# Optimization experiments

Hardware: AMD Instinct MI355X
Metric: run time of the kernel (lower is better)

## Reference

```python
import jax, jax.numpy as jnp
import numpy as np

N_CLUSTERS = 64
N_GHOST = 2
EPS = 1e-12  # F.normalize eps


def setup_inputs() -> dict:
    key = jax.random.key(0)
    k1, k2, k3, k4 = jax.random.split(key, 4)
    n_utts, feat_dim, duration = 16, 256, 1500
    x = jax.random.normal(k1, (n_utts, feat_dim, duration), dtype=jnp.float32)
    centroids = jax.random.uniform(k2, (N_CLUSTERS, feat_dim), dtype=jnp.float32)
    # NetVLAD init ties linear.weight = 2*alpha*centroids(+ghosts); here independent params suffice for a math baseline
    lin_w = jax.random.normal(k3, (N_CLUSTERS + N_GHOST, feat_dim), dtype=jnp.float32)
    lin_b = jax.random.normal(k4, (N_CLUSTERS + N_GHOST,), dtype=jnp.float32)
    return {"x": x, "centroids": centroids, "lin_w": lin_w, "lin_b": lin_b}


def reference(x, centroids, lin_w, lin_b):
    # x: [u, f, t] -> [u, t, f]
    n_utts = x.shape[0]
    xt = jnp.transpose(x, (0, 2, 1))
    # soft assignments over clusters+ghosts, then drop ghost columns
    logits = jnp.einsum('utf,cf->utc', xt, lin_w) + lin_b  # [u,t,C+G]
    a = jax.nn.softmax(logits, axis=2)[..., :N_CLUSTERS]   # [u,t,C]
    # Fused NetVLAD aggregation (algebraically identical to
    # sum_t a[u,t,c] * (x[u,t,:] - centroids[c,:]) without materializing
    # the [u,t,C,f] residual tensor):
    comp = jnp.einsum('utc,utf->ucf', a, xt) - a.sum(axis=1)[..., None] * centroids  # [u,C,f]
    # intra-normalization (F.normalize p=2 over feat dim)
    comp = comp / jnp.maximum(jnp.linalg.norm(comp, axis=2, keepdims=True), EPS)
    sv = comp.reshape(n_utts, -1)  # [u, C*f]
    sv = sv / jnp.maximum(jnp.linalg.norm(sv, axis=1, keepdims=True), EPS)
    return sv
```

## Files before the change

### kernel.cpp

```cpp
#include <hip/hip_runtime.h>
#include <math.h>


#define NU 16
#define NF 256
#define NT 1500
#define NC 64
#define NCG 66
#define EPSN 1e-12f

#define T_CHUNK 96
#define N_CHUNKS 16

__device__ __forceinline__ float blk_reduce_sum(float v, float* sbuf) {
    #pragma unroll
    for (int off = 32; off > 0; off >>= 1) v += __shfl_down(v, off, 64);
    const int lane = threadIdx.x & 63, wv = threadIdx.x >> 6;
    if (lane == 0) sbuf[wv] = v;
    __syncthreads();
    float r = sbuf[0] + sbuf[1] + sbuf[2] + sbuf[3];
    __syncthreads();
    return r;
}

__global__ __launch_bounds__(256) void k1_assign(
        const float* __restrict__ x, const float* __restrict__ lin_w,
        const float* __restrict__ lin_b, float* __restrict__ a_ws) {
    const int u    = blockIdx.y;
    const int t0   = blockIdx.x * 64;
    const int tid  = threadIdx.x;
    const int lane = tid & 63;
    const int wave = tid >> 6;
    const int t    = t0 + lane;
    const int tc   = (t < NT) ? t : (NT - 1);

    __shared__ float wsm[4][NCG][16];
    __shared__ float red[2][NCG][64];

    float acc[NCG];
    #pragma unroll
    for (int c = 0; c < NCG; ++c) acc[c] = 0.0f;

    for (int fc = 0; fc < 4; ++fc) {
        const int fbase = wave * 64 + fc * 16;
        for (int idx = lane; idx < NCG * 16; idx += 64) {
            const int c = idx >> 4, k = idx & 15;
            wsm[wave][c][k] = lin_w[c * NF + fbase + k];
        }
        __syncthreads();

        float xv[16];
        #pragma unroll
        for (int k = 0; k < 16; ++k)
            xv[k] = x[(u * NF + fbase + k) * NT + tc];

        #pragma unroll
        for (int c = 0; c < NCG; ++c) {
            const float4* wr = (const float4*)(&wsm[wave][c][0]);
            const float4 w0 = wr[0], w1 = wr[1], w2 = wr[2], w3 = wr[3];
            acc[c] += w0.x*xv[0]  + w0.y*xv[1]  + w0.z*xv[2]  + w0.w*xv[3]
                    + w1.x*xv[4]  + w1.y*xv[5]  + w1.z*xv[6]  + w1.w*xv[7]
                    + w2.x*xv[8]  + w2.y*xv[9]  + w2.z*xv[10] + w2.w*xv[11]
                    + w3.x*xv[12] + w3.y*xv[13] + w3.z*xv[14] + w3.w*xv[15];
        }
        __syncthreads();
    }

    if (wave >= 2) {
        #pragma unroll
        for (int c = 0; c < NCG; ++c) red[wave - 2][c][lane] = acc[c];
    }
    __syncthreads();
    if (wave < 2) {
        #pragma unroll
        for (int c = 0; c < NCG; ++c) acc[c] += red[wave][c][lane];
    }
    __syncthreads();
    if (wave == 1) {
        #pragma unroll
        for (int c = 0; c < NCG; ++c) red[0][c][lane] = acc[c];
    }
    __syncthreads();
    if (wave == 0) {
        #pragma unroll
        for (int c = 0; c < NCG; ++c) acc[c] += red[0][c][lane] + lin_b[c];
        float m = -INFINITY;
        #pragma unroll
        for (int c = 0; c < NCG; ++c) m = fmaxf(m, acc[c]);
        float s = 0.0f;
        #pragma unroll
        for (int c = 0; c < NCG; ++c) { acc[c] = __expf(acc[c] - m); s += acc[c]; }
        const float inv = 1.0f / s;
        if (t < NT) {
            #pragma unroll
            for (int c = 0; c < NC; ++c)
                a_ws[(u * NC + c) * NT + t] = acc[c] * inv;
        }
    }
}

__global__ __launch_bounds__(256) void k2_agg(
        const float* __restrict__ x, const float* __restrict__ a_ws,
        float* __restrict__ partial) {
    const int u = blockIdx.y, chunk = blockIdx.x;
    const int tid = threadIdx.x;
    const int t0 = chunk * T_CHUNK;
    const int t_end = min(t0 + T_CHUNK, NT);

    __shared__ float Asm[64][17];
    __shared__ float Xsm[256][17];

    float acc[8][8];
    #pragma unroll
    for (int i = 0; i < 8; ++i)
        #pragma unroll
        for (int j = 0; j < 8; ++j) acc[i][j] = 0.0f;

    const int cs = tid >> 2;
    const int ks = (tid & 3) * 4;
    const int c_base = (tid >> 5) * 8;
    const int fl = tid & 31;

    for (int k0 = t0; k0 < t_end; k0 += 16) {
        const int rem = t_end - k0;
        {
            const float* rp = a_ws + (u * NC + cs) * NT + k0 + ks;
            float4 v;
            if (ks + 3 < rem) v = *(const float4*)rp;
            else {
                v.x = (ks + 0 < rem) ? rp[0] : 0.0f;
                v.y = (ks + 1 < rem) ? rp[1] : 0.0f;
                v.z = (ks + 2 < rem) ? rp[2] : 0.0f;
                v.w = (ks + 3 < rem) ? rp[3] : 0.0f;
            }
            Asm[cs][ks+0] = v.x; Asm[cs][ks+1] = v.y;
            Asm[cs][ks+2] = v.z; Asm[cs][ks+3] = v.w;
        }
        #pragma unroll
        for (int r = 0; r < 4; ++r) {
            const int f = cs + 64 * r;
            const float* rp = x + (u * NF + f) * NT + k0 + ks;
            float4 v;
            if (ks + 3 < rem) v = *(const float4*)rp;
            else {
                v.x = (ks + 0 < rem) ? rp[0] : 0.0f;
                v.y = (ks + 1 < rem) ? rp[1] : 0.0f;
                v.z = (ks + 2 < rem) ? rp[2] : 0.0f;
                v.w = (ks + 3 < rem) ? rp[3] : 0.0f;
            }
            Xsm[f][ks+0] = v.x; Xsm[f][ks+1] = v.y;
            Xsm[f][ks+2] = v.z; Xsm[f][ks+3] = v.w;
        }
        __syncthreads();

        #pragma unroll 4
        for (int k = 0; k < 16; ++k) {
            float av[8], xv[8];
            #pragma unroll
            for (int i = 0; i < 8; ++i) av[i] = Asm[c_base + i][k];
            #pragma unroll
            for (int j = 0; j < 8; ++j) xv[j] = Xsm[fl + 32 * j][k];
            #pragma unroll
            for (int i = 0; i < 8; ++i)
                #pragma unroll
                for (int j = 0; j < 8; ++j) acc[i][j] += av[i] * xv[j];
        }
        __syncthreads();
    }

    #pragma unroll
    for (int i = 0; i < 8; ++i) {
        const int c = c_base + i;
        float* op = partial + ((chunk * NU + u) * NC + c) * NF;
        #pragma unroll
        for (int j = 0; j < 8; ++j) op[fl + 32 * j] = acc[i][j];
    }
}

__global__ __launch_bounds__(256) void k3_norm(
        const float* __restrict__ a_ws, const float* __restrict__ partial,
        const float* __restrict__ centroids, float* __restrict__ compn,
        float* __restrict__ rowsq) {
    const int c = blockIdx.x, u = blockIdx.y;
    const int tid = threadIdx.x;
    __shared__ float sbuf[4];

    float s = 0.0f;
    const float* arow = a_ws + (u * NC + c) * NT;
    for (int i = tid; i < NT; i += 256) s += arow[i];
    const float asum = blk_reduce_sum(s, sbuf);

    float val = 0.0f;
    #pragma unroll
    for (int ch = 0; ch < N_CHUNKS; ++ch)
        val += partial[((ch * NU + u) * NC + c) * NF + tid];
    val -= asum * centroids[c * NF + tid];

    const float ss = blk_reduce_sum(val * val, sbuf);
    const float d  = fmaxf(sqrtf(ss), EPSN);
    compn[(u * NC + c) * NF + tid] = val / d;
    if (tid == 0) rowsq[u * NC + c] = ss / (d * d);
}

__global__ __launch_bounds__(256) void k4_scale(
        const float* __restrict__ compn, const float* __restrict__ rowsq,
        float* __restrict__ out) {
    const int u = blockIdx.y;
    const int tid = threadIdx.x;
    float gss = 0.0f;
    #pragma unroll
    for (int cc = 0; cc < NC; ++cc) gss += rowsq[u * NC + cc];
    const float inv = 1.0f / fmaxf(sqrtf(gss), EPSN);
    const int base = u * (NC * NF) + blockIdx.x * 4096;
    #pragma unroll
    for (int r = 0; r < 16; ++r) {
        const int idx = base + r * 256 + tid;
        out[idx] = compn[idx] * inv;
    }
}

extern "C" void kernel_launch(void* const* d_in, const int* in_sizes, int n_in,
                              void* d_out, int out_size, void* d_ws, size_t ws_size,
                              hipStream_t stream) {
    (void)in_sizes; (void)n_in; (void)out_size; (void)ws_size;
    const float* x         = (const float*)d_in[0];
    const float* centroids = (const float*)d_in[1];
    const float* lin_w     = (const float*)d_in[2];
    const float* lin_b     = (const float*)d_in[3];
    float* out = (float*)d_out;

    float* ws      = (float*)d_ws;
    float* a_ws    = ws;
    float* partial = a_ws + NU * NC * NT;
    float* compn   = partial + N_CHUNKS * NU * NC * NF;
    float* rowsq   = compn + NU * NC * NF;

    dim3 blk(256);
    hipLaunchKernelGGL(k1_assign, dim3(24, NU), blk, 0, stream, x, lin_w, lin_b, a_ws);
    hipLaunchKernelGGL(k2_agg,    dim3(N_CHUNKS, NU), blk, 0, stream, x, a_ws, partial);
    hipLaunchKernelGGL(k3_norm,   dim3(NC, NU), blk, 0, stream, a_ws, partial, centroids, compn, rowsq);
    hipLaunchKernelGGL(k4_scale,  dim3(4, NU), blk, 0, stream, compn, rowsq, out);
}
```

Baseline: 140.4 us.

## Fuse all NetVLAD stages into one cooperative kernel with grid syncs

Replaces the four kernel launches with a single cooperative kernel. Each block loads its x chunk into shared memory once, computes the softmax assignments into shared memory, and aggregates them without writing the assignment tensor to global memory. Assignment sums are accumulated during aggregation, and the normalization and scaling stages follow after grid syncs. This removes launch overhead and the global round trip of the assignment tensor, but it limits the grid to 256 blocks at one block per CU and adds grid-sync cost.

```diff
diff --git a/kernel.cpp b/kernel.cpp
--- a/kernel.cpp
+++ b/kernel.cpp
@@ -1,6 +1,9 @@
 #include <hip/hip_runtime.h>
+#include <hip/hip_cooperative_groups.h>
 #include <math.h>
 
+
+namespace cg = cooperative_groups;
 
 #define NU 16
 #define NF 256
@@ -8,9 +11,9 @@
 #define NC 64
 #define NCG 66
 #define EPSN 1e-12f
-
-#define T_CHUNK 96
-#define N_CHUNKS 16
+#define TCH 96
+#define NCHUNK 16
+#define XPAD 97
 
 __device__ __forceinline__ float blk_reduce_sum(float v, float* sbuf) {
     #pragma unroll
@@ -23,23 +26,17 @@
     return r;
 }
 
-__global__ __launch_bounds__(256) void k1_assign(
-        const float* __restrict__ x, const float* __restrict__ lin_w,
-        const float* __restrict__ lin_b, float* __restrict__ a_ws) {
-    const int u    = blockIdx.y;
-    const int t0   = blockIdx.x * 64;
-    const int tid  = threadIdx.x;
-    const int lane = tid & 63;
-    const int wave = tid >> 6;
-    const int t    = t0 + lane;
-    const int tc   = (t < NT) ? t : (NT - 1);
-
-    __shared__ float wsm[4][NCG][16];
-    __shared__ float red[2][NCG][64];
-
+__device__ __forceinline__ void logits_pass(
+        const float* __restrict__ lin_w, const float* __restrict__ lin_b,
+        const float (*Xsm)[XPAD], float (*Asm)[XPAD], float* scratch,
+        const int wave, const int lane, const int kbase, const int nstore,
+        const int t0) {
     float acc[NCG];
     #pragma unroll
     for (int c = 0; c < NCG; ++c) acc[c] = 0.0f;
+
+    const int kk = min(kbase + lane, TCH - 1);
+    float (*wsm)[NCG][16] = (float (*)[NCG][16])scratch;
 
     for (int fc = 0; fc < 4; ++fc) {
         const int fbase = wave * 64 + fc * 16;
@@ -48,12 +45,9 @@
             wsm[wave][c][k] = lin_w[c * NF + fbase + k];
         }
         __syncthreads();
-
         float xv[16];
         #pragma unroll
-        for (int k = 0; k < 16; ++k)
-            xv[k] = x[(u * NF + fbase + k) * NT + tc];
-
+        for (int k = 0; k < 16; ++k) xv[k] = Xsm[fbase + k][kk];
         #pragma unroll
         for (int c = 0; c < NCG; ++c) {
             const float4* wr = (const float4*)(&wsm[wave][c][0]);
@@ -66,6 +60,7 @@
         __syncthreads();
     }
 
+    float (*red)[NCG][64] = (float (*)[NCG][64])scratch;
     if (wave >= 2) {
         #pragma unroll
         for (int c = 0; c < NCG; ++c) red[wave - 2][c][lane] = acc[c];
@@ -90,132 +85,141 @@
         float s = 0.0f;
         #pragma unroll
         for (int c = 0; c < NCG; ++c) { acc[c] = __expf(acc[c] - m); s += acc[c]; }
-        const float inv = 1.0f / s;
-        if (t < NT) {
-            #pragma unroll
-            for (int c = 0; c < NC; ++c)
-                a_ws[(u * NC + c) * NT + t] = acc[c] * inv;
-        }
-    }
-}
-
-__global__ __launch_bounds__(256) void k2_agg(
-        const float* __restrict__ x, const float* __restrict__ a_ws,
-        float* __restrict__ partial) {
-    const int u = blockIdx.y, chunk = blockIdx.x;
-    const int tid = threadIdx.x;
-    const int t0 = chunk * T_CHUNK;
-    const int t_end = min(t0 + T_CHUNK, NT);
-
-    __shared__ float Asm[64][17];
-    __shared__ float Xsm[256][17];
-
-    float acc[8][8];
-    #pragma unroll
-    for (int i = 0; i < 8; ++i)
-        #pragma unroll
-        for (int j = 0; j < 8; ++j) acc[i][j] = 0.0f;
-
-    const int cs = tid >> 2;
-    const int ks = (tid & 3) * 4;
-    const int c_base = (tid >> 5) * 8;
-    const int fl = tid & 31;
-
-    for (int k0 = t0; k0 < t_end; k0 += 16) {
-        const int rem = t_end - k0;
-        {
-            const float* rp = a_ws + (u * NC + cs) * NT + k0 + ks;
-            float4 v;
-            if (ks + 3 < rem) v = *(const float4*)rp;
-            else {
-                v.x = (ks + 0 < rem) ? rp[0] : 0.0f;
-                v.y = (ks + 1 < rem) ? rp[1] : 0.0f;
-                v.z = (ks + 2 < rem) ? rp[2] : 0.0f;
-                v.w = (ks + 3 < rem) ? rp[3] : 0.0f;
+        const int t = t0 + kbase + lane;
+        const float scale = (t < NT) ? (1.0f / s) : 0.0f;
+        if (lane < nstore) {
+            #pragma unroll
+            for (int c = 0; c < NC; ++c) Asm[c][kbase + lane] = acc[c] * scale;
+        }
+    }
+    __syncthreads();
+}
+
+__global__ __launch_bounds__(256, 1) void fused_netvlad(
+        const float* __restrict__ x, const float* __restrict__ centroids,
+        const float* __restrict__ lin_w, const float* __restrict__ lin_b,
+        float* __restrict__ partial, float* __restrict__ asum_part,
+        float* __restrict__ compn, float* __restrict__ rowsq,
+        float* __restrict__ out) {
+    __shared__ float Xsm[NF][XPAD];
+    __shared__ float Asm[NC][XPAD];
+    __shared__ float scratch[2 * NCG * 64];
+    __shared__ float sbuf[4];
+
+    cg::grid_group grid = cg::this_grid();
+
+    const int chunk = blockIdx.x, u = blockIdx.y;
+    const int tid  = threadIdx.x;
+    const int lane = tid & 63, wave = tid >> 6;
+    const int t0 = chunk * TCH;
+
+    {
+        const int cs = tid >> 2;
+        const int ks = (tid & 3) * 4;
+        #pragma unroll
+        for (int k0 = 0; k0 < TCH; k0 += 16) {
+            #pragma unroll
+            for (int r = 0; r < 4; ++r) {
+                const int f  = cs + 64 * r;
+                const int kk = k0 + ks;
+                const int tg = t0 + kk;
+                const float* rp = x + ((size_t)(u * NF + f)) * NT + tg;
+                float4 v;
+                if (tg + 3 < NT) v = *(const float4*)rp;
+                else {
+                    v.x = (tg + 0 < NT) ? rp[0] : 0.0f;
+                    v.y = (tg + 1 < NT) ? rp[1] : 0.0f;
+                    v.z = (tg + 2 < NT) ? rp[2] : 0.0f;
+                    v.w = (tg + 3 < NT) ? rp[3] : 0.0f;
+                }
+                Xsm[f][kk+0] = v.x; Xsm[f][kk+1] = v.y;
+                Xsm[f][kk+2] = v.z; Xsm[f][kk+3] = v.w;
             }
-            Asm[cs][ks+0] = v.x; Asm[cs][ks+1] = v.y;
-            Asm[cs][ks+2] = v.z; Asm[cs][ks+3] = v.w;
-        }
-        #pragma unroll
-        for (int r = 0; r < 4; ++r) {
-            const int f = cs + 64 * r;
-            const float* rp = x + (u * NF + f) * NT + k0 + ks;
-            float4 v;
-            if (ks + 3 < rem) v = *(const float4*)rp;
-            else {
-                v.x = (ks + 0 < rem) ? rp[0] : 0.0f;
-                v.y = (ks + 1 < rem) ? rp[1] : 0.0f;
-                v.z = (ks + 2 < rem) ? rp[2] : 0.0f;
-                v.w = (ks + 3 < rem) ? rp[3] : 0.0f;
+        }
+    }
+    __syncthreads();
+
+    logits_pass(lin_w, lin_b, Xsm, Asm, scratch, wave, lane, 0, 64, t0);
+    logits_pass(lin_w, lin_b, Xsm, Asm, scratch, wave, lane, 64, 32, t0);
+
+    {
+        float aggacc[8][8];
+        float asacc[8];
+        #pragma unroll
+        for (int i = 0; i < 8; ++i) {
+            asacc[i] = 0.0f;
+            #pragma unroll
+            for (int j = 0; j < 8; ++j) aggacc[i][j] = 0.0f;
+        }
+        const int c_base = (tid >> 5) * 8;
+        const int fl = tid & 31;
+
+        #pragma unroll 4
+        for (int k = 0; k < TCH; ++k) {
+            float av[8], xv[8];
+            #pragma unroll
+            for (int i = 0; i < 8; ++i) av[i] = Asm[c_base + i][k];
+            #pragma unroll
+            for (int j = 0; j < 8; ++j) xv[j] = Xsm[fl + 32 * j][k];
+            #pragma unroll
+            for (int i = 0; i < 8; ++i) {
+                asacc[i] += av[i];
+                #pragma unroll
+                for (int j = 0; j < 8; ++j) aggacc[i][j] += av[i] * xv[j];
             }
-            Xsm[f][ks+0] = v.x; Xsm[f][ks+1] = v.y;
-            Xsm[f][ks+2] = v.z; Xsm[f][ks+3] = v.w;
-        }
-        __syncthreads();
-
-        #pragma unroll 4
-        for (int k = 0; k < 16; ++k) {
-            float av[8], xv[8];
-            #pragma unroll
-            for (int i = 0; i < 8; ++i) av[i] = Asm[c_base + i][k];
-            #pragma unroll
-            for (int j = 0; j < 8; ++j) xv[j] = Xsm[fl + 32 * j][k];
+        }
+
+        #pragma unroll
+        for (int i = 0; i < 8; ++i) {
+            float* op = partial + ((size_t)((chunk * NU + u) * NC + c_base + i)) * NF;
+            #pragma unroll
+            for (int j = 0; j < 8; ++j) op[fl + 32 * j] = aggacc[i][j];
+        }
+        if (fl == 0) {
             #pragma unroll
             for (int i = 0; i < 8; ++i)
-                #pragma unroll
-                for (int j = 0; j < 8; ++j) acc[i][j] += av[i] * xv[j];
-        }
-        __syncthreads();
-    }
-
-    #pragma unroll
-    for (int i = 0; i < 8; ++i) {
-        const int c = c_base + i;
-        float* op = partial + ((chunk * NU + u) * NC + c) * NF;
-        #pragma unroll
-        for (int j = 0; j < 8; ++j) op[fl + 32 * j] = acc[i][j];
-    }
-}
-
-__global__ __launch_bounds__(256) void k3_norm(
-        const float* __restrict__ a_ws, const float* __restrict__ partial,
-        const float* __restrict__ centroids, float* __restrict__ compn,
-        float* __restrict__ rowsq) {
-    const int c = blockIdx.x, u = blockIdx.y;
-    const int tid = threadIdx.x;
-    __shared__ float sbuf[4];
-
-    float s = 0.0f;
-    const float* arow = a_ws + (u * NC + c) * NT;
-    for (int i = tid; i < NT; i += 256) s += arow[i];
-    const float asum = blk_reduce_sum(s, sbuf);
-
-    float val = 0.0f;
-    #pragma unroll
-    for (int ch = 0; ch < N_CHUNKS; ++ch)
-        val += partial[((ch * NU + u) * NC + c) * NF + tid];
-    val -= asum * centroids[c * NF + tid];
-
-    const float ss = blk_reduce_sum(val * val, sbuf);
-    const float d  = fmaxf(sqrtf(ss), EPSN);
-    compn[(u * NC + c) * NF + tid] = val / d;
-    if (tid == 0) rowsq[u * NC + c] = ss / (d * d);
-}
-
-__global__ __launch_bounds__(256) void k4_scale(
-        const float* __restrict__ compn, const float* __restrict__ rowsq,
-        float* __restrict__ out) {
-    const int u = blockIdx.y;
-    const int tid = threadIdx.x;
-    float gss = 0.0f;
-    #pragma unroll
-    for (int cc = 0; cc < NC; ++cc) gss += rowsq[u * NC + cc];
-    const float inv = 1.0f / fmaxf(sqrtf(gss), EPSN);
-    const int base = u * (NC * NF) + blockIdx.x * 4096;
-    #pragma unroll
-    for (int r = 0; r < 16; ++r) {
-        const int idx = base + r * 256 + tid;
-        out[idx] = compn[idx] * inv;
+                asum_part[(chunk * NU + u) * NC + c_base + i] = asacc[i];
+        }
+    }
+
+    __threadfence();
+    grid.sync();
+
+    const int B = blockIdx.y * gridDim.x + blockIdx.x;
+    for (int task = 0; task < 4; ++task) {
+        const int tix = B * 4 + task;
+        const int uu = tix >> 6, cc = tix & 63;
+
+        float asum = 0.0f;
+        #pragma unroll
+        for (int ch = 0; ch < NCHUNK; ++ch)
+            asum += asum_part[(ch * NU + uu) * NC + cc];
+
+        float val = 0.0f;
+        #pragma unroll
+        for (int ch = 0; ch < NCHUNK; ++ch)
+            val += partial[((size_t)((ch * NU + uu) * NC + cc)) * NF + tid];
+        val -= asum * centroids[cc * NF + tid];
+
+        const float ss = blk_reduce_sum(val * val, sbuf);
+        const float d  = fmaxf(sqrtf(ss), EPSN);
+        compn[((size_t)(uu * NC + cc)) * NF + tid] = val / d;
+        if (tid == 0) rowsq[uu * NC + cc] = ss / (d * d);
+    }
+
+    __threadfence();
+    grid.sync();
+
+    {
+        const int uu = B >> 4, sl = B & 15;
+        float gss = 0.0f;
+        #pragma unroll
+        for (int c2 = 0; c2 < NC; ++c2) gss += rowsq[uu * NC + c2];
+        const float inv = 1.0f / fmaxf(sqrtf(gss), EPSN);
+        const int base = uu * (NC * NF) + sl * 1024 + tid * 4;
+        float4 v = *(const float4*)(compn + base);
+        v.x *= inv; v.y *= inv; v.z *= inv; v.w *= inv;
+        *(float4*)(out + base) = v;
     }
 }
 
@@ -229,15 +233,15 @@
     const float* lin_b     = (const float*)d_in[3];
     float* out = (float*)d_out;
 
-    float* ws      = (float*)d_ws;
-    float* a_ws    = ws;
-    float* partial = a_ws + NU * NC * NT;
-    float* compn   = partial + N_CHUNKS * NU * NC * NF;
-    float* rowsq   = compn + NU * NC * NF;
-
-    dim3 blk(256);
-    hipLaunchKernelGGL(k1_assign, dim3(24, NU), blk, 0, stream, x, lin_w, lin_b, a_ws);
-    hipLaunchKernelGGL(k2_agg,    dim3(N_CHUNKS, NU), blk, 0, stream, x, a_ws, partial);
-    hipLaunchKernelGGL(k3_norm,   dim3(NC, NU), blk, 0, stream, a_ws, partial, centroids, compn, rowsq);
-    hipLaunchKernelGGL(k4_scale,  dim3(4, NU), blk, 0, stream, compn, rowsq, out);
-}
+    float* ws        = (float*)d_ws;
+    float* partial   = ws;
+    float* asum_part = partial + (size_t)NCHUNK * NU * NC * NF;
+    float* compn     = asum_part + NCHUNK * NU * NC;
+    float* rowsq     = compn + NU * NC * NF;
+
+    void* args[] = {(void*)&x, (void*)&centroids, (void*)&lin_w, (void*)&lin_b,
+                    (void*)&partial, (void*)&asum_part, (void*)&compn,
+                    (void*)&rowsq, (void*)&out};
+    hipLaunchCooperativeKernel((const void*)fused_netvlad,
+                               dim3(NCHUNK, NU), dim3(256), args, 0, stream);
+}
```

Result: slower. 286.5 us (+104.0%).
